# Performance work log

Hardware: AMD Instinct MI355X
Metric: run time of the kernel (lower is better)

Reference implementation:

```python
import jax, jax.numpy as jnp
import numpy as np

N_NODES = 50000
N_EDGES = 600000
DIM = 128
N_REL = 3
LN_EPS = 1e-5


def setup_inputs() -> dict:
    key = jax.random.key(0)
    ks = jax.random.split(key, 8)
    x = jax.random.normal(ks[0], (N_NODES, DIM), dtype=jnp.float32)
    edge_index = jax.random.randint(ks[1], (2, N_EDGES), 0, N_NODES, dtype=jnp.int64)
    edge_type = jax.random.randint(ks[2], (N_EDGES,), 0, N_REL, dtype=jnp.int64)
    # learned params
    relation_weights = jax.random.normal(ks[3], (N_REL, DIM, DIM), dtype=jnp.float32)
    lim = 1.0 / np.sqrt(DIM)
    lin_w = jax.random.uniform(ks[4], (DIM, DIM), dtype=jnp.float32, minval=-lim, maxval=lim)
    lin_b = jax.random.uniform(ks[5], (DIM,), dtype=jnp.float32, minval=-lim, maxval=lim)
    ln_gamma = jnp.ones((DIM,), dtype=jnp.float32)
    ln_beta = jnp.zeros((DIM,), dtype=jnp.float32)
    return {"x": x, "edge_index": edge_index, "edge_type": edge_type,
            "relation_weights": relation_weights, "lin_w": lin_w, "lin_b": lin_b,
            "ln_gamma": ln_gamma, "ln_beta": ln_beta}


def reference(x, edge_index, edge_type, relation_weights, lin_w, lin_b, ln_gamma, ln_beta):
    # x: [N, D]; edge_index: [2, E]; edge_type: [E]
    N = x.shape[0]
    src, dst = edge_index[0], edge_index[1]
    xs = x[src]  # gather: [E, D]
    # relation-wise masked GEMM accumulated into per-edge messages
    msg = jnp.zeros_like(xs)
    for r in range(relation_weights.shape[0]):  # small fixed relation loop
        mask = (edge_type == r)[:, None]
        msg = msg + jnp.where(mask, xs @ relation_weights[r], jnp.zeros((), x.dtype))
    agg = jax.ops.segment_sum(msg, dst, num_segments=N)  # scatter-add: [N, D]
    deg = jax.ops.segment_sum(jnp.ones_like(dst, dtype=x.dtype), dst, num_segments=N)
    deg = jnp.maximum(deg, 1.0)
    out = agg / deg[:, None]
    # linear + residual + LayerNorm (eps 1e-5, biased variance)
    h = x @ lin_w.T + lin_b + out
    mu = jnp.mean(h, axis=-1, keepdims=True)
    var = jnp.mean((h - mu) ** 2, axis=-1, keepdims=True)
    return ln_gamma * (h - mu) * jax.lax.rsqrt(var + LN_EPS) + ln_beta
```

## Files before the change

kernel.cpp:

```cpp
#include <hip/hip_runtime.h>

#define DIM    128
#define NREL   3
#define KS     (NREL*DIM)
#define NB     16
#define LN_EPS 1e-5f
#define PPART  32
#define KSLOT  24
#define PW     (PPART*KSLOT)
#define OVFCAP 2048
#define CH     256
#define GPREP  256

typedef unsigned int uint;
typedef unsigned char uchar;
typedef float f32x4 __attribute__((ext_vector_type(4)));
typedef short short8 __attribute__((ext_vector_type(8)));

__device__ __forceinline__ unsigned short f2bf(float f) {
    union { float f; uint u; } c; c.f = f;
    return (unsigned short)((c.u + 0x7fffu + ((c.u >> 16) & 1u)) >> 16);
}
__device__ __forceinline__ uint packbf(float a, float b) {
    return (uint)f2bf(a) | ((uint)f2bf(b) << 16);
}
__device__ __forceinline__ float blo(uint u) {
    union { uint u; float f; } c; c.u = u << 16; return c.f;
}
__device__ __forceinline__ float bhi(uint u) {
    union { uint u; float f; } c; c.u = u & 0xffff0000u; return c.f;
}
__device__ __forceinline__ int ldidx(const int* p, size_t i, int i64) {
    return i64 ? p[2*i] : p[i];
}
__device__ __forceinline__ int fo(int m, int k) {
    return ((k >> 5) << 6) + ((((k >> 3) & 3)) << 4) + m;
}
__device__ __forceinline__ int SW(int s) { return s ^ ((s >> 4) & 7); }

__device__ __forceinline__ void block_probe(const int* __restrict__ ei, int t, int* s_i64) {
    if (t < 64) {
        int z = 0;
        #pragma unroll
        for (int i = 0; i < 4; i++) z += (ei[t*4 + i] == 0) ? 1 : 0;
        #pragma unroll
        for (int off = 1; off < 64; off <<= 1) z += __shfl_xor(z, off);
        if (t == 0) *s_i64 = (z > 64) ? 1 : 0;
    }
}

__device__ __forceinline__ void bpack_work(int idx, const float* __restrict__ relw,
                                           const float* __restrict__ linw,
                                           unsigned short* __restrict__ Bpack) {
    if (idx < 8192) {
        int lane = idx & 63, kk = (idx >> 6) & 15, tile = idx >> 10;
        int q = lane >> 4, n = tile * 16 + (lane & 15);
        uint vv[4];
        #pragma unroll
        for (int jp = 0; jp < 4; jp++) {
            int k0 = kk * 32 + q * 8 + jp * 2;
            float v0 = (k0     < KS) ? relw[(size_t)k0*DIM + n]
                                     : linw[(size_t)n*DIM + (k0 - KS)];
            float v1 = (k0 + 1 < KS) ? relw[(size_t)(k0+1)*DIM + n]
                                     : linw[(size_t)n*DIM + (k0 + 1 - KS)];
            vv[jp] = packbf(v0, v1);
        }
        uint4 v; v.x = vv[0]; v.y = vv[1]; v.z = vv[2]; v.w = vv[3];
        ((uint4*)Bpack)[idx] = v;
    }
}

__global__ __launch_bounds__(1024)
void prep_kernel(const int* __restrict__ ei, const int* __restrict__ et,
                 const float* __restrict__ x, int E, int N, int Ee, int NBIN,
                 uchar* __restrict__ cnt, int* __restrict__ binbuf,
                 int* __restrict__ ovf_cnt, int2* __restrict__ ovf,
                 const float* __restrict__ relw, const float* __restrict__ linw,
                 unsigned short* __restrict__ Bpack, unsigned short* __restrict__ xbf)
{
    extern __shared__ int lhist[];
    __shared__ int s_i64;
    const int b = blockIdx.x, t = threadIdx.x;

    if (b < PPART) {
        block_probe(ei, t, &s_i64);
        for (int i = t; i < NBIN; i += 1024) lhist[i] = 0;
        __syncthreads();
        const int i64 = s_i64;
        const int e0 = b * Ee;
        const int e1 = min(E, e0 + Ee);
        for (int e = e0 + t; e < e1; e += 1024) {
            int s = ldidx(ei, (size_t)e, i64);
            int d = ldidx(ei, (size_t)E + e, i64);
            int r = ldidx(et, (size_t)e, i64);
            int bin = d >> 4;
            int tag = s | ((d & 15) << 20) | (r << 24);
            int lr = atomicAdd(&lhist[bin], 1);
            if (lr < KSLOT) {
                binbuf[bin * PW + b * KSLOT + lr] = tag;
            } else {
                int oi = atomicAdd(ovf_cnt, 1);
                if (oi < OVFCAP) ovf[oi] = make_int2(tag, bin);
            }
        }
        __syncthreads();
        for (int i = t; i < NBIN; i += 1024)
            cnt[i * PPART + b] = (uchar)min(lhist[i], KSLOT);
    } else {
        const int cb = b - PPART;
        const int nconv = GPREP - PPART;
        const float4* x4 = (const float4*)x;
        const int items = N * (DIM / 8);
        for (int i = cb * 1024 + t; i < items; i += nconv * 1024) {
            float4 a = x4[i*2], bb = x4[i*2 + 1];
            uint4 v;
            v.x = packbf(a.x, a.y); v.y = packbf(a.z, a.w);
            v.z = packbf(bb.x, bb.y); v.w = packbf(bb.z, bb.w);
            ((uint4*)xbf)[i] = v;
        }
        bpack_work(cb * 1024 + t, relw, linw, Bpack);
    }
}

__global__ __launch_bounds__(256)
void main_kernel(const unsigned short* __restrict__ xbf,
                 const uchar* __restrict__ cnt,
                 const int* __restrict__ binbuf,
                 const int* __restrict__ ovf_cnt, const int2* __restrict__ ovf,
                 const unsigned short* __restrict__ Bpack,
                 const float* __restrict__ linb,
                 const float* __restrict__ gamma,
                 const float* __restrict__ beta,
                 float* __restrict__ out, int N)
{
    __shared__ uint4 Af[1024];
    __shared__ int s_tag[CH];
    __shared__ int s_cmp[CH];
    __shared__ int s_cnt[48];
    __shared__ int s_off[49];
    __shared__ int s_cur[48];
    __shared__ int s_coff[PPART + 1];
    __shared__ int s_n;
    __shared__ float s_mu[NB], s_rs[NB];

    const int t  = threadIdx.x;
    const int bb = blockIdx.x;
    const int n0 = bb * NB;
    const int m  = t >> 4;
    const int c  = t & 15;
    const int n  = n0 + m;

    const uint4* xh = (const uint4*)xbf;

    float a0[8], a1[8], a2[8];
    #pragma unroll
    for (int i = 0; i < 8; i++) { a0[i] = 0.f; a1[i] = 0.f; a2[i] = 0.f; }
    int deg = 0;
    uint4 res = {0,0,0,0};
    if (n < N) res = xh[(size_t)n*16 + c];

    if (t < 64) {
        int cv = (t < PPART) ? (int)cnt[(size_t)bb * PPART + t] : 0;
        int v = cv;
        #pragma unroll
        for (int off = 1; off < PPART; off <<= 1) {
            int u = __shfl_up(v, off);
            if (t >= off) v += u;
        }
        if (t < PPART) s_coff[t + 1] = v;
        if (t == 0) s_coff[0] = 0;
    }
    __syncthreads();

    #define PROCESS_CHUNK(NC) { \
        const int nc_ = (NC); \
        if (t < 48) s_cnt[t] = 0; \
        __syncthreads(); \
        int key_ = -1; \
        if (t < nc_) { \
            int tg_ = s_tag[t]; \
            key_ = (((tg_ >> 20) & 15) * 3) + ((tg_ >> 24) & 3); \
            atomicAdd(&s_cnt[key_], 1); \
        } \
        __syncthreads(); \
        if (t < 64) { \
            int cv_ = (t < 48) ? s_cnt[t] : 0; \
            int v_ = cv_; \
            _Pragma("unroll") \
            for (int off = 1; off < 64; off <<= 1) { \
                int u_ = __shfl_up(v_, off); \
                if (t >= off) v_ += u_; \
            } \
            if (t < 48) { s_off[t + 1] = v_; s_cur[t] = v_ - cv_; } \
            if (t == 0) s_off[0] = 0; \
        } \
        __syncthreads(); \
        if (t < nc_) { \
            int pos_ = atomicAdd(&s_cur[key_], 1); \
            s_cmp[pos_] = s_tag[t] & 0xFFFFF; \
        } \
        __syncthreads(); \
        deg += s_off[m*3 + 3] - s_off[m*3]; \
        { \
            int p_ = s_off[m*3 + 0], pe_ = s_off[m*3 + 1]; \
            GATH(a0) \
            p_ = s_off[m*3 + 1]; pe_ = s_off[m*3 + 2]; \
            GATH(a1) \
            p_ = s_off[m*3 + 2]; pe_ = s_off[m*3 + 3]; \
            GATH(a2) \
        } \
        __syncthreads(); }

    #define GATH(ACC) \
        for (; p_ + 3 < pe_; p_ += 4) { \
            int s0 = s_cmp[p_],   s1 = s_cmp[p_+1]; \
            int s2 = s_cmp[p_+2], s3 = s_cmp[p_+3]; \
            uint4 g0 = xh[(size_t)s0*16 + c], g1 = xh[(size_t)s1*16 + c]; \
            uint4 g2 = xh[(size_t)s2*16 + c], g3 = xh[(size_t)s3*16 + c]; \
            ACC[0] += blo(g0.x)+blo(g1.x)+blo(g2.x)+blo(g3.x); \
            ACC[1] += bhi(g0.x)+bhi(g1.x)+bhi(g2.x)+bhi(g3.x); \
            ACC[2] += blo(g0.y)+blo(g1.y)+blo(g2.y)+blo(g3.y); \
            ACC[3] += bhi(g0.y)+bhi(g1.y)+bhi(g2.y)+bhi(g3.y); \
            ACC[4] += blo(g0.z)+blo(g1.z)+blo(g2.z)+blo(g3.z); \
            ACC[5] += bhi(g0.z)+bhi(g1.z)+bhi(g2.z)+bhi(g3.z); \
            ACC[6] += blo(g0.w)+blo(g1.w)+blo(g2.w)+blo(g3.w); \
            ACC[7] += bhi(g0.w)+bhi(g1.w)+bhi(g2.w)+bhi(g3.w); \
        } \
        for (; p_ < pe_; ++p_) { \
            int s0 = s_cmp[p_]; \
            uint4 g0 = xh[(size_t)s0*16 + c]; \
            ACC[0] += blo(g0.x); ACC[1] += bhi(g0.x); \
            ACC[2] += blo(g0.y); ACC[3] += bhi(g0.y); \
            ACC[4] += blo(g0.z); ACC[5] += bhi(g0.z); \
            ACC[6] += blo(g0.w); ACC[7] += bhi(g0.w); \
        }

    int g0 = 0;
    while (g0 < PPART) {
        const int base0 = s_coff[g0];
        int gend = g0;
        while (gend < PPART && s_coff[gend + 1] - base0 <= CH) ++gend;
        const int nc = s_coff[gend] - base0;
        if (t < nc) {
            int cell = g0;
            while (s_coff[cell + 1] - base0 <= t) ++cell;
            int slot = t - (s_coff[cell] - base0);
            s_tag[t] = binbuf[(size_t)bb * PW + cell * KSLOT + slot];
        }
        PROCESS_CHUNK(nc)
        g0 = gend;
    }

    {
        int L = min(ovf_cnt[0], OVFCAP);
        if (L > 0) {
            if (t == 0) s_n = 0;
            __syncthreads();
            for (int i = t; i < L; i += 256) {
                int2 o = ovf[i];
                if (o.y == bb) {
                    int pos = atomicAdd(&s_n, 1);
                    if (pos < CH) s_tag[pos] = o.x;
                }
            }
            __syncthreads();
            int nc = min(s_n, CH);
            PROCESS_CHUNK(nc)
        }
    }
    #undef GATH
    #undef PROCESS_CHUNK

    {
        float inv = 1.0f / fmaxf((float)deg, 1.0f);
        uint4 w0;
        w0.x = packbf(a0[0]*inv, a0[1]*inv); w0.y = packbf(a0[2]*inv, a0[3]*inv);
        w0.z = packbf(a0[4]*inv, a0[5]*inv); w0.w = packbf(a0[6]*inv, a0[7]*inv);
        Af[SW(fo(m, 0*DIM + 8*c))] = w0;
        w0.x = packbf(a1[0]*inv, a1[1]*inv); w0.y = packbf(a1[2]*inv, a1[3]*inv);
        w0.z = packbf(a1[4]*inv, a1[5]*inv); w0.w = packbf(a1[6]*inv, a1[7]*inv);
        Af[SW(fo(m, 1*DIM + 8*c))] = w0;
        w0.x = packbf(a2[0]*inv, a2[1]*inv); w0.y = packbf(a2[2]*inv, a2[3]*inv);
        w0.z = packbf(a2[4]*inv, a2[5]*inv); w0.w = packbf(a2[6]*inv, a2[7]*inv);
        Af[SW(fo(m, 2*DIM + 8*c))] = w0;
        Af[SW(fo(m, KS + 8*c))] = res;
    }
    __syncthreads();

    const int lane = t & 63;
    const int w    = t >> 6;
    const int mm   = lane & 15;
    const int q    = lane >> 4;
    f32x4 acc0 = {0,0,0,0}, acc1 = {0,0,0,0};
    {
        const short8* Aq = (const short8*)Af;
        const short8* Bq = (const short8*)Bpack;
        #pragma unroll
        for (int kk = 0; kk < 16; kk++) {
            short8 a  = Aq[SW(kk*64 + lane)];
            short8 b0 = Bq[((w*2 + 0)*16 + kk)*64 + lane];
            short8 b1 = Bq[((w*2 + 1)*16 + kk)*64 + lane];
            acc0 = __builtin_amdgcn_mfma_f32_16x16x32_bf16(a, b0, acc0, 0, 0, 0);
            acc1 = __builtin_amdgcn_mfma_f32_16x16x32_bf16(a, b1, acc1, 0, 0, 0);
        }
    }
    __syncthreads();

    float* H = (float*)Af;
    {
        int rb = q * 4;
        #pragma unroll
        for (int nt = 0; nt < 2; nt++) {
            int d = (w*2 + nt)*16 + mm;
            float lb = linb[d];
            f32x4 a = (nt == 0) ? acc0 : acc1;
            #pragma unroll
            for (int i = 0; i < 4; i++)
                H[(rb + i)*132 + d] = a[i] + lb;
        }
    }
    __syncthreads();

    {
        int j = t >> 4, p = t & 15;
        float s1 = 0.f, s2 = 0.f;
        const float* hr = &H[j*132 + p*8];
        #pragma unroll
        for (int i = 0; i < 8; i++) { float v = hr[i]; s1 += v; s2 += v*v; }
        #pragma unroll
        for (int off = 1; off < 16; off <<= 1) {
            s1 += __shfl_xor(s1, off);
            s2 += __shfl_xor(s2, off);
        }
        if (p == 0) {
            float mu  = s1 * (1.0f/DIM);
            float var = s2 * (1.0f/DIM) - mu*mu;
            s_mu[j] = mu;
            s_rs[j] = rsqrtf(var + LN_EPS);
        }
    }
    __syncthreads();

    {
        int d  = t & 127;
        int jb = (t >> 7) * 8;
        float g = gamma[d];
        float b = beta[d];
        #pragma unroll
        for (int jj = 0; jj < 8; jj++) {
            int j = jb + jj;
            int nn = n0 + j;
            if (nn < N) {
                float hv = H[j*132 + d];
                out[(size_t)nn*DIM + d] = g * (hv - s_mu[j]) * s_rs[j] + b;
            }
        }
    }
}

extern "C" void kernel_launch(void* const* d_in, const int* in_sizes, int n_in,
                              void* d_out, int out_size, void* d_ws, size_t ws_size,
                              hipStream_t stream)
{
    const float* x   = (const float*)d_in[0];
    const int*   ei  = (const int*)d_in[1];
    const int*   et  = (const int*)d_in[2];
    const float* rw  = (const float*)d_in[3];
    const float* lw  = (const float*)d_in[4];
    const float* lb  = (const float*)d_in[5];
    const float* lg  = (const float*)d_in[6];
    const float* lbe = (const float*)d_in[7];

    const int N    = in_sizes[0] / DIM;
    const int E    = in_sizes[2];
    const int NBIN = (N + NB - 1) / NB;
    const int Ee   = (E + PPART - 1) / PPART;

    char* wp = (char*)d_ws;
    int*  ovf_cnt = (int*)wp;             wp += 16;
    int2* ovf     = (int2*)wp;            wp += (size_t)OVFCAP * 8;
    uchar* cnt    = (uchar*)wp;           wp += ((size_t)NBIN * PPART + 63) & ~(size_t)63;
    int*  binbuf  = (int*)wp;             wp += (size_t)NBIN * PW * 4;
    unsigned short* Bpack = (unsigned short*)wp;   wp += 512 * 128 * 2;
    unsigned short* xbf   = (unsigned short*)wp;   wp += (size_t)N * DIM * 2;
    (void)ws_size;

    hipMemsetAsync(ovf_cnt, 0, 4, stream);
    prep_kernel<<<GPREP, 1024, (size_t)NBIN * 4, stream>>>(ei, et, x, E, N, Ee, NBIN,
                                                           cnt, binbuf, ovf_cnt, ovf,
                                                           rw, lw, Bpack, xbf);
    main_kernel<<<NBIN, 256, 0, stream>>>(xbf, cnt, binbuf, ovf_cnt, ovf, Bpack,
                                          lb, lg, lbe, (float*)d_out, N);
}
```

Measured before the change: 183.7 us.

## Split edge binning across more smaller blocks and streamline per-chunk tag sorting

The edge-binning pass now uses three times as many partitions (96 instead of 32) with fewer slots per bin cell, and runs on 256-thread blocks, so more blocks share the edge scan. The overflow buffer grows to absorb the extra cells that exceed the smaller slot count. In the main kernel, an LDS cell map replaces the per-thread linear search for each tag's source cell, and tag counting is folded into the binbuf load so the chunk no longer stages tags through shared memory. In exchange, the cell prefix sum becomes an LDS scan with many barriers, and more edges may go through the slower overflow path.

Measured after the change: 192.5 us. +4.8%, slower.

```diff
diff --git a/kernel.cpp b/kernel.cpp
--- a/kernel.cpp
+++ b/kernel.cpp
@@ -5,12 +5,12 @@
 #define KS     (NREL*DIM)
 #define NB     16
 #define LN_EPS 1e-5f
-#define PPART  32
-#define KSLOT  24
+#define PPART  96
+#define KSLOT  8
 #define PW     (PPART*KSLOT)
-#define OVFCAP 2048
+#define OVFCAP 16384
 #define CH     256
-#define GPREP  256
+#define GPREP  352
 
 typedef unsigned int uint;
 typedef unsigned char uchar;
@@ -70,7 +70,7 @@
     }
 }
 
-__global__ __launch_bounds__(1024)
+__global__ __launch_bounds__(256)
 void prep_kernel(const int* __restrict__ ei, const int* __restrict__ et,
                  const float* __restrict__ x, int E, int N, int Ee, int NBIN,
                  uchar* __restrict__ cnt, int* __restrict__ binbuf,
@@ -84,12 +84,12 @@
 
     if (b < PPART) {
         block_probe(ei, t, &s_i64);
-        for (int i = t; i < NBIN; i += 1024) lhist[i] = 0;
+        for (int i = t; i < NBIN; i += 256) lhist[i] = 0;
         __syncthreads();
         const int i64 = s_i64;
         const int e0 = b * Ee;
         const int e1 = min(E, e0 + Ee);
-        for (int e = e0 + t; e < e1; e += 1024) {
+        for (int e = e0 + t; e < e1; e += 256) {
             int s = ldidx(ei, (size_t)e, i64);
             int d = ldidx(ei, (size_t)E + e, i64);
             int r = ldidx(et, (size_t)e, i64);
@@ -104,21 +104,21 @@
             }
         }
         __syncthreads();
-        for (int i = t; i < NBIN; i += 1024)
+        for (int i = t; i < NBIN; i += 256)
             cnt[i * PPART + b] = (uchar)min(lhist[i], KSLOT);
     } else {
         const int cb = b - PPART;
         const int nconv = GPREP - PPART;
         const float4* x4 = (const float4*)x;
         const int items = N * (DIM / 8);
-        for (int i = cb * 1024 + t; i < items; i += nconv * 1024) {
+        for (int i = cb * 256 + t; i < items; i += nconv * 256) {
             float4 a = x4[i*2], bb = x4[i*2 + 1];
             uint4 v;
             v.x = packbf(a.x, a.y); v.y = packbf(a.z, a.w);
             v.z = packbf(bb.x, bb.y); v.w = packbf(bb.z, bb.w);
             ((uint4*)xbf)[i] = v;
         }
-        bpack_work(cb * 1024 + t, relw, linw, Bpack);
+        bpack_work(cb * 256 + t, relw, linw, Bpack);
     }
 }
 
@@ -136,6 +136,7 @@
     __shared__ uint4 Af[1024];
     __shared__ int s_tag[CH];
     __shared__ int s_cmp[CH];
+    __shared__ int s_map[CH];
     __shared__ int s_cnt[48];
     __shared__ int s_off[49];
     __shared__ int s_cur[48];
@@ -159,30 +160,19 @@
     uint4 res = {0,0,0,0};
     if (n < N) res = xh[(size_t)n*16 + c];
 
-    if (t < 64) {
-        int cv = (t < PPART) ? (int)cnt[(size_t)bb * PPART + t] : 0;
-        int v = cv;
-        #pragma unroll
-        for (int off = 1; off < PPART; off <<= 1) {
-            int u = __shfl_up(v, off);
-            if (t >= off) v += u;
-        }
+    if (t < PPART) s_coff[t + 1] = (int)cnt[(size_t)bb * PPART + t];
+    if (t == 0) s_coff[0] = 0;
+    __syncthreads();
+    for (int off = 1; off < PPART; off <<= 1) {
+        int v = 0;
+        if (t < PPART) { v = s_coff[t + 1]; if (t >= off) v += s_coff[t + 1 - off]; }
+        __syncthreads();
         if (t < PPART) s_coff[t + 1] = v;
-        if (t == 0) s_coff[0] = 0;
-    }
-    __syncthreads();
-
-    #define PROCESS_CHUNK(NC) { \
+        __syncthreads();
+    }
+
+    #define FINISH_CHUNK(NC) { \
         const int nc_ = (NC); \
-        if (t < 48) s_cnt[t] = 0; \
-        __syncthreads(); \
-        int key_ = -1; \
-        if (t < nc_) { \
-            int tg_ = s_tag[t]; \
-            key_ = (((tg_ >> 20) & 15) * 3) + ((tg_ >> 24) & 3); \
-            atomicAdd(&s_cnt[key_], 1); \
-        } \
-        __syncthreads(); \
         if (t < 64) { \
             int cv_ = (t < 48) ? s_cnt[t] : 0; \
             int v_ = cv_; \
@@ -196,8 +186,8 @@
         } \
         __syncthreads(); \
         if (t < nc_) { \
-            int pos_ = atomicAdd(&s_cur[key_], 1); \
-            s_cmp[pos_] = s_tag[t] & 0xFFFFF; \
+            int pos_ = atomicAdd(&s_cur[key], 1); \
+            s_cmp[pos_] = tg & 0xFFFFF; \
         } \
         __syncthreads(); \
         deg += s_off[m*3 + 3] - s_off[m*3]; \
@@ -241,13 +231,22 @@
         int gend = g0;
         while (gend < PPART && s_coff[gend + 1] - base0 <= CH) ++gend;
         const int nc = s_coff[gend] - base0;
+        if (t < 48) s_cnt[t] = 0;
+        for (int cell = g0 + t; cell < gend; cell += 256) {
+            int lo = s_coff[cell] - base0, hi = s_coff[cell + 1] - base0;
+            for (int s2 = lo; s2 < hi; ++s2) s_map[s2] = cell;
+        }
+        __syncthreads();
+        int key = -1, tg = 0;
         if (t < nc) {
-            int cell = g0;
-            while (s_coff[cell + 1] - base0 <= t) ++cell;
+            int cell = s_map[t];
             int slot = t - (s_coff[cell] - base0);
-            s_tag[t] = binbuf[(size_t)bb * PW + cell * KSLOT + slot];
-        }
-        PROCESS_CHUNK(nc)
+            tg = binbuf[(size_t)bb * PW + cell * KSLOT + slot];
+            key = (((tg >> 20) & 15) * 3) + ((tg >> 24) & 3);
+            atomicAdd(&s_cnt[key], 1);
+        }
+        __syncthreads();
+        FINISH_CHUNK(nc)
         g0 = gend;
     }
 
@@ -255,6 +254,7 @@
         int L = min(ovf_cnt[0], OVFCAP);
         if (L > 0) {
             if (t == 0) s_n = 0;
+            if (t < 48) s_cnt[t] = 0;
             __syncthreads();
             for (int i = t; i < L; i += 256) {
                 int2 o = ovf[i];
@@ -265,11 +265,18 @@
             }
             __syncthreads();
             int nc = min(s_n, CH);
-            PROCESS_CHUNK(nc)
+            int key = -1, tg = 0;
+            if (t < nc) {
+                tg = s_tag[t];
+                key = (((tg >> 20) & 15) * 3) + ((tg >> 24) & 3);
+                atomicAdd(&s_cnt[key], 1);
+            }
+            __syncthreads();
+            FINISH_CHUNK(nc)
         }
     }
     #undef GATH
-    #undef PROCESS_CHUNK
+    #undef FINISH_CHUNK
 
     {
         float inv = 1.0f / fmaxf((float)deg, 1.0f);
@@ -386,9 +393,9 @@
     (void)ws_size;
 
     hipMemsetAsync(ovf_cnt, 0, 4, stream);
-    prep_kernel<<<GPREP, 1024, (size_t)NBIN * 4, stream>>>(ei, et, x, E, N, Ee, NBIN,
-                                                           cnt, binbuf, ovf_cnt, ovf,
-                                                           rw, lw, Bpack, xbf);
+    prep_kernel<<<GPREP, 256, (size_t)NBIN * 4, stream>>>(ei, et, x, E, N, Ee, NBIN,
+                                                          cnt, binbuf, ovf_cnt, ovf,
+                                                          rw, lw, Bpack, xbf);
     main_kernel<<<NBIN, 256, 0, stream>>>(xbf, cnt, binbuf, ovf_cnt, ovf, Bpack,
                                           lb, lg, lbe, (float*)d_out, N);
 }
```
